# Kernel optimization log

Hardware: AMD Instinct MI355X
Metric: run time of the kernel (lower is better)

## Reference

```python
import jax, jax.numpy as jnp
import numpy as np

N_NODES = 8192
N_EDGES = 262144
D_FEAT = 512
NHID = 32
LATENT = 16


def setup_inputs() -> dict:
    key = jax.random.key(0)
    ks = jax.random.split(key, 12)
    inp = {
        "features": jax.random.normal(ks[0], (N_NODES, D_FEAT), dtype=jnp.float32),
        "edge_src": jax.random.randint(ks[1], (N_EDGES,), 0, N_NODES, dtype=jnp.int32),
        "edge_dst": jax.random.randint(ks[2], (N_EDGES,), 0, N_NODES, dtype=jnp.int32),
        "edge_weight": jax.random.uniform(ks[3], (N_EDGES,), dtype=jnp.float32),
        # GCEncoder params (GCNConv: out = A @ (x W) + b)
        "Wg1": jax.random.normal(ks[4], (D_FEAT, NHID), dtype=jnp.float32) / np.sqrt(D_FEAT),
        "bg1": jnp.zeros((NHID,), jnp.float32),
        "Wg2": jax.random.normal(ks[5], (NHID, LATENT), dtype=jnp.float32) / np.sqrt(NHID),
        "bg2": jnp.zeros((LATENT,), jnp.float32),
        # MLP encoder params
        "We1": jax.random.normal(ks[6], (D_FEAT, NHID), dtype=jnp.float32) / np.sqrt(D_FEAT),
        "be1": jnp.zeros((NHID,), jnp.float32),
        "We2": jax.random.normal(ks[7], (NHID, LATENT), dtype=jnp.float32) / np.sqrt(NHID),
        "be2": jnp.zeros((LATENT,), jnp.float32),
        # MLP decoder params (latent -> features)
        "Wd1": jax.random.normal(ks[8], (LATENT, NHID), dtype=jnp.float32) / np.sqrt(LATENT),
        "bd1": jnp.zeros((NHID,), jnp.float32),
        "Wd2": jax.random.normal(ks[9], (NHID, D_FEAT), dtype=jnp.float32) / np.sqrt(NHID),
        "bd2": jnp.zeros((D_FEAT,), jnp.float32),
    }
    return inp


def _gcn_conv(x, W, b, edge_src, edge_dst, edge_weight, n_nodes):
    # transform then sparse aggregate: A @ (x W) + b
    xw = x @ W                                   # [N, out]
    msg = xw[edge_src] * edge_weight[:, None]    # [E, out]
    agg = jax.ops.segment_sum(msg, edge_dst, num_segments=n_nodes)
    return agg + b


def reference(features, edge_src, edge_dst, edge_weight,
              Wg1, bg1, Wg2, bg2, We1, be1, We2, be2, Wd1, bd1, Wd2, bd2):
    n = features.shape[0]
    # GCEncoder (dropout p=0.0)
    h = jax.nn.relu(_gcn_conv(features, Wg1, bg1, edge_src, edge_dst, edge_weight, n))
    za = jax.nn.relu(_gcn_conv(h, Wg2, bg2, edge_src, edge_dst, edge_weight, n))
    # MLP encoder
    zx = jax.nn.relu(jax.nn.relu(features @ We1 + be1) @ We2 + be2)
    # concat latents
    z = jnp.concatenate([za, zx], axis=1)        # [N, 2*latent]
    # inner-product decoder: sigmoid(z z^T)  -> [N, N]
    adj_recon = jax.nn.sigmoid(z @ z.T)
    # feature decoder MLP
    feat_recon = jax.nn.relu(jax.nn.relu(zx @ Wd1 + bd1) @ Wd2 + bd2)
    return adj_recon, feat_recon, z
```

## Files before the change

kernel.cpp:

```cpp
#include <hip/hip_runtime.h>

typedef unsigned short ushort_t;
typedef __attribute__((ext_vector_type(8))) short short8;
typedef __attribute__((ext_vector_type(4))) float floatx4;

#define N_NODES 8192
#define N_EDGES 262144
#define D_FEAT 512
#define NHID 32
#define LATENT 16

#define ADJ_OFF 0
#define FEAT_OFF (8192*8192)
#define Z_OFF (8192*8192 + 8192*512)

static __device__ __forceinline__ ushort_t f2bf(float f) {
    unsigned int u = __float_as_uint(f);
    unsigned int r = u + 0x7fffu + ((u >> 16) & 1u);
    return (ushort_t)(r >> 16);
}

__global__ __launch_bounds__(256) void k_zero(int* counts) {
    int i = blockIdx.x * 256 + threadIdx.x;
    if (i < N_NODES) counts[i] = 0;
}

__global__ __launch_bounds__(256) void k_hist(const int* edst, int* counts) {
    int e = blockIdx.x * 256 + threadIdx.x;
    atomicAdd(&counts[edst[e]], 1);
}

__global__ __launch_bounds__(1024) void k_scan(const int* counts, int* offs, int* cursor) {
    __shared__ int sdata[1024];
    int t = threadIdx.x;
    int base = t * 8;
    int c[8], local[8];
    int s = 0;
    #pragma unroll
    for (int j = 0; j < 8; j++) { c[j] = counts[base + j]; }
    #pragma unroll
    for (int j = 0; j < 8; j++) { local[j] = s; s += c[j]; }
    sdata[t] = s;
    __syncthreads();
    for (int off = 1; off < 1024; off <<= 1) {
        int v = sdata[t];
        int add = (t >= off) ? sdata[t - off] : 0;
        __syncthreads();
        sdata[t] = v + add;
        __syncthreads();
    }
    int excl = (t == 0) ? 0 : sdata[t - 1];
    #pragma unroll
    for (int j = 0; j < 8; j++) {
        int o = excl + local[j];
        offs[base + j] = o;
        cursor[base + j] = o;
    }
}

__global__ __launch_bounds__(256) void k_scatter(const int* esrc, const int* edst,
                                                 const float* ew, int* cursor,
                                                 int* ssrc, float* sw) {
    int e = blockIdx.x * 256 + threadIdx.x;
    int d = edst[e];
    int pos = atomicAdd(&cursor[d], 1);
    ssrc[pos] = esrc[e];
    sw[pos] = ew[e];
}

__global__ __launch_bounds__(256) void k_enc(const float* feat, const float* Wg1,
                                             const float* We1, const float* be1,
                                             const float* We2, const float* be2,
                                             float* xwg, float* zxf) {
    __shared__ float WL[64][64];
    __shared__ float FL[32][68];
    __shared__ float HE[32][33];
    int tid = threadIdx.x;
    int n = tid >> 3;
    int c0 = (tid & 7) * 8;
    int m0 = blockIdx.x * 32;
    float acc[8];
    #pragma unroll
    for (int j = 0; j < 8; j++) acc[j] = 0.f;

    for (int kt = 0; kt < 8; kt++) {
        __syncthreads();
        for (int i = tid; i < 4096; i += 256) {
            int k = i >> 6, c = i & 63;
            int kg = kt * 64 + k;
            WL[k][c] = (c < 32) ? Wg1[kg * 32 + c] : We1[kg * 32 + (c - 32)];
        }
        {
            const float* src = feat + (m0 + n) * 512 + kt * 64 + c0;
            float4 v0 = *(const float4*)(src);
            float4 v1 = *(const float4*)(src + 4);
            *(float4*)&FL[n][c0] = v0;
            *(float4*)&FL[n][c0 + 4] = v1;
        }
        __syncthreads();
        #pragma unroll 4
        for (int k = 0; k < 64; k++) {
            float a = FL[n][k];
            float4 w0 = *(const float4*)&WL[k][c0];
            float4 w1 = *(const float4*)&WL[k][c0 + 4];
            acc[0] += a * w0.x; acc[1] += a * w0.y;
            acc[2] += a * w0.z; acc[3] += a * w0.w;
            acc[4] += a * w1.x; acc[5] += a * w1.y;
            acc[6] += a * w1.z; acc[7] += a * w1.w;
        }
    }
    if ((tid & 7) < 4) {
        #pragma unroll
        for (int j = 0; j < 8; j++) xwg[(m0 + n) * 32 + c0 + j] = acc[j];
    } else {
        int h0 = c0 - 32;
        #pragma unroll
        for (int j = 0; j < 8; j++) {
            float v = acc[j] + be1[h0 + j];
            HE[n][h0 + j] = v > 0.f ? v : 0.f;
        }
    }
    __syncthreads();
    int j0 = (tid & 7) * 2;
    #pragma unroll
    for (int jj = 0; jj < 2; jj++) {
        int j = j0 + jj;
        float s = be2[j];
        #pragma unroll 8
        for (int cc = 0; cc < 32; cc++) s += HE[n][cc] * We2[cc * 16 + j];
        zxf[(m0 + n) * 16 + j] = s > 0.f ? s : 0.f;
    }
}

__global__ __launch_bounds__(256) void k_agg1(const float* xwg, const int* offs,
                                              const int* counts, const int* ssrc,
                                              const float* sw, const float* bg1,
                                              const float* Wg2, float* hw2) {
    __shared__ float hsh[8][33];
    int ln = threadIdx.x >> 5, c = threadIdx.x & 31;
    int n = blockIdx.x * 8 + ln;
    int st = offs[n], en = st + counts[n];
    float acc = 0.f;
    for (int i = st; i < en; i++) {
        acc += sw[i] * xwg[ssrc[i] * 32 + c];
    }
    float h = acc + bg1[c];
    hsh[ln][c] = h > 0.f ? h : 0.f;
    __syncthreads();
    if (threadIdx.x < 128) {
        int l2 = threadIdx.x >> 4, j = threadIdx.x & 15;
        float s2 = 0.f;
        #pragma unroll 8
        for (int cc = 0; cc < 32; cc++) s2 += hsh[l2][cc] * Wg2[cc * 16 + j];
        hw2[(blockIdx.x * 8 + l2) * 16 + j] = s2;
    }
}

__global__ __launch_bounds__(256) void k_agg2(const float* hw2, const int* offs,
                                              const int* counts, const int* ssrc,
                                              const float* sw, const float* bg2,
                                              const float* zxf, ushort_t* zbf,
                                              float* zout) {
    int ln = threadIdx.x >> 4, c = threadIdx.x & 15;
    int n = blockIdx.x * 16 + ln;
    int st = offs[n], en = st + counts[n];
    float acc = 0.f;
    for (int i = st; i < en; i++) {
        acc += sw[i] * hw2[ssrc[i] * 16 + c];
    }
    float za = acc + bg2[c];
    za = za > 0.f ? za : 0.f;
    float zx = zxf[n * 16 + c];
    zout[n * 32 + c] = za;
    zout[n * 32 + 16 + c] = zx;
    zbf[n * 32 + c] = f2bf(za);
    zbf[n * 32 + 16 + c] = f2bf(zx);
}

__global__ __launch_bounds__(256) void k_feat1(const float* zxf, const float* Wd1,
                                               const float* bd1, float* tf) {
    int gid = blockIdx.x * 256 + threadIdx.x;
    int n = gid >> 5, c = gid & 31;
    float s = bd1[c];
    #pragma unroll
    for (int k = 0; k < 16; k++) s += zxf[n * 16 + k] * Wd1[k * 32 + c];
    tf[gid] = s > 0.f ? s : 0.f;
}

__global__ __launch_bounds__(256) void k_feat2(const float* tf, const float* Wd2,
                                               const float* bd2, float* outF) {
    int n = blockIdx.x;
    int c = threadIdx.x * 2;
    float s0 = bd2[c], s1 = bd2[c + 1];
    #pragma unroll 8
    for (int k = 0; k < 32; k++) {
        float t = tf[n * 32 + k];
        s0 += t * Wd2[k * 512 + c];
        s1 += t * Wd2[k * 512 + c + 1];
    }
    s0 = s0 > 0.f ? s0 : 0.f;
    s1 = s1 > 0.f ? s1 : 0.f;
    float2 pk = make_float2(s0, s1);
    *(float2*)(outF + n * 512 + c) = pk;
}

__global__ __launch_bounds__(256) void k_adj(const ushort_t* zbf, float* out) {
    int l = threadIdx.x & 63;
    int wv = threadIdx.x >> 6;
    int strip = blockIdx.x & 15;
    int rtg = blockIdx.x >> 4;
    int rt = rtg * 4 + wv;
    int q = l >> 4, cl = l & 15;
    int m0 = rt * 16, c0 = strip * 512;
    short8 a = *(const short8*)(zbf + (m0 + cl) * 32 + q * 8);
    for (int p = 0; p < 16; p++) {
        int colA = c0 + p * 32 + 2 * cl;
        short8 bA = *(const short8*)(zbf + colA * 32 + q * 8);
        short8 bB = *(const short8*)(zbf + (colA + 1) * 32 + q * 8);
        floatx4 accA = {0,0,0,0}, accB = {0,0,0,0};
        accA = __builtin_amdgcn_mfma_f32_16x16x32_bf16(a, bA, accA, 0, 0, 0);
        accB = __builtin_amdgcn_mfma_f32_16x16x32_bf16(a, bB, accB, 0, 0, 0);
        #pragma unroll
        for (int r = 0; r < 4; r++) {
            int row = m0 + q * 4 + r;
            float sA = 1.f / (1.f + __expf(-accA[r]));
            float sB = 1.f / (1.f + __expf(-accB[r]));
            float2 pk = make_float2(sA, sB);
            *(float2*)(out + (size_t)row * 8192 + colA) = pk;
        }
    }
}

extern "C" void kernel_launch(void* const* d_in, const int* in_sizes, int n_in,
                              void* d_out, int out_size, void* d_ws, size_t ws_size,
                              hipStream_t stream) {
    const float* feat = (const float*)d_in[0];
    const int* esrc = (const int*)d_in[1];
    const int* edst = (const int*)d_in[2];
    const float* ew = (const float*)d_in[3];
    const float* Wg1 = (const float*)d_in[4];
    const float* bg1 = (const float*)d_in[5];
    const float* Wg2 = (const float*)d_in[6];
    const float* bg2 = (const float*)d_in[7];
    const float* We1 = (const float*)d_in[8];
    const float* be1 = (const float*)d_in[9];
    const float* We2 = (const float*)d_in[10];
    const float* be2 = (const float*)d_in[11];
    const float* Wd1 = (const float*)d_in[12];
    const float* bd1 = (const float*)d_in[13];
    const float* Wd2 = (const float*)d_in[14];
    const float* bd2 = (const float*)d_in[15];
    float* out = (float*)d_out;

    char* ws = (char*)d_ws;
    float* xwg      = (float*)(ws + 0);
    float* zxf      = (float*)(ws + 1048576);
    float* hw2      = (float*)(ws + 1572864);
    ushort_t* zbf   = (ushort_t*)(ws + 2097152);
    float* tf       = (float*)(ws + 2621440);
    int* counts     = (int*)(ws + 3670016);
    int* offs       = (int*)(ws + 3702784);
    int* cursor     = (int*)(ws + 3735552);
    int* ssrc       = (int*)(ws + 3768320);
    float* sw       = (float*)(ws + 4816896);

    k_zero<<<32, 256, 0, stream>>>(counts);
    k_hist<<<N_EDGES / 256, 256, 0, stream>>>(edst, counts);
    k_scan<<<1, 1024, 0, stream>>>(counts, offs, cursor);
    k_scatter<<<N_EDGES / 256, 256, 0, stream>>>(esrc, edst, ew, cursor, ssrc, sw);
    k_enc<<<N_NODES / 32, 256, 0, stream>>>(feat, Wg1, We1, be1, We2, be2, xwg, zxf);
    k_agg1<<<N_NODES / 8, 256, 0, stream>>>(xwg, offs, counts, ssrc, sw, bg1, Wg2, hw2);
    k_agg2<<<N_NODES / 16, 256, 0, stream>>>(hw2, offs, counts, ssrc, sw, bg2, zxf,
                                             zbf, out + Z_OFF);
    k_feat1<<<N_NODES * 32 / 256, 256, 0, stream>>>(zxf, Wd1, bd1, tf);
    k_feat2<<<N_NODES, 256, 0, stream>>>(tf, Wd2, bd2, out + FEAT_OFF);
    k_adj<<<(N_NODES / 16 / 4) * 16, 256, 0, stream>>>(zbf, out + ADJ_OFF);
}
```

Baseline: 473.7 us.

## Pack edges, fuse feature decoder, widen adj stores with nontemporal writes

Packs edge source index and weight into one int2 array and unrolls the aggregation loops by four. Re-tiles the encoder GEMM and fuses the two feature-decoder kernels into one block that processes 16 nodes, writing with nontemporal stores. The adjacency kernel now computes four MFMA tiles per step so it can emit float4 nontemporal stores to the 256 MB output, aiming to improve write efficiency. Adds __restrict__ throughout; the trade-off is more registers per thread and more code complexity.

```diff
diff --git a/kernel.cpp b/kernel.cpp
--- a/kernel.cpp
+++ b/kernel.cpp
@@ -3,6 +3,7 @@
 typedef unsigned short ushort_t;
 typedef __attribute__((ext_vector_type(8))) short short8;
 typedef __attribute__((ext_vector_type(4))) float floatx4;
+typedef __attribute__((ext_vector_type(2))) float floatx2;
 
 #define N_NODES 8192
 #define N_EDGES 262144
@@ -20,17 +21,18 @@
     return (ushort_t)(r >> 16);
 }
 
-__global__ __launch_bounds__(256) void k_zero(int* counts) {
+__global__ __launch_bounds__(256) void k_zero(int* __restrict__ counts) {
     int i = blockIdx.x * 256 + threadIdx.x;
     if (i < N_NODES) counts[i] = 0;
 }
 
-__global__ __launch_bounds__(256) void k_hist(const int* edst, int* counts) {
+__global__ __launch_bounds__(256) void k_hist(const int* __restrict__ edst, int* __restrict__ counts) {
     int e = blockIdx.x * 256 + threadIdx.x;
     atomicAdd(&counts[edst[e]], 1);
 }
 
-__global__ __launch_bounds__(1024) void k_scan(const int* counts, int* offs, int* cursor) {
+__global__ __launch_bounds__(1024) void k_scan(const int* __restrict__ counts,
+                                               int* __restrict__ offs, int* __restrict__ cursor) {
     __shared__ int sdata[1024];
     int t = threadIdx.x;
     int base = t * 8;
@@ -58,91 +60,119 @@
     }
 }
 
-__global__ __launch_bounds__(256) void k_scatter(const int* esrc, const int* edst,
-                                                 const float* ew, int* cursor,
-                                                 int* ssrc, float* sw) {
+__global__ __launch_bounds__(256) void k_scatter(const int* __restrict__ esrc,
+                                                 const int* __restrict__ edst,
+                                                 const float* __restrict__ ew,
+                                                 int* __restrict__ cursor,
+                                                 int2* __restrict__ sedge) {
     int e = blockIdx.x * 256 + threadIdx.x;
     int d = edst[e];
     int pos = atomicAdd(&cursor[d], 1);
-    ssrc[pos] = esrc[e];
-    sw[pos] = ew[e];
-}
-
-__global__ __launch_bounds__(256) void k_enc(const float* feat, const float* Wg1,
-                                             const float* We1, const float* be1,
-                                             const float* We2, const float* be2,
-                                             float* xwg, float* zxf) {
-    __shared__ float WL[64][64];
-    __shared__ float FL[32][68];
+    sedge[pos] = make_int2(esrc[e], __float_as_int(ew[e]));
+}
+
+__global__ __launch_bounds__(256) void k_enc(const float* __restrict__ feat,
+                                             const float* __restrict__ Wg1,
+                                             const float* __restrict__ We1,
+                                             const float* __restrict__ be1,
+                                             const float* __restrict__ We2,
+                                             const float* __restrict__ be2,
+                                             float* __restrict__ xwg,
+                                             float* __restrict__ zxf) {
+    __shared__ float WL[32][64];
+    __shared__ float FL[32][33];
     __shared__ float HE[32][33];
     int tid = threadIdx.x;
-    int n = tid >> 3;
-    int c0 = (tid & 7) * 8;
+    int cr = tid & 15;
+    int nr = tid >> 4;
     int m0 = blockIdx.x * 32;
-    float acc[8];
-    #pragma unroll
-    for (int j = 0; j < 8; j++) acc[j] = 0.f;
-
-    for (int kt = 0; kt < 8; kt++) {
+    float acc[2][4] = {};
+
+    for (int kt = 0; kt < 16; kt++) {
         __syncthreads();
-        for (int i = tid; i < 4096; i += 256) {
-            int k = i >> 6, c = i & 63;
-            int kg = kt * 64 + k;
-            WL[k][c] = (c < 32) ? Wg1[kg * 32 + c] : We1[kg * 32 + (c - 32)];
-        }
         {
-            const float* src = feat + (m0 + n) * 512 + kt * 64 + c0;
-            float4 v0 = *(const float4*)(src);
-            float4 v1 = *(const float4*)(src + 4);
-            *(float4*)&FL[n][c0] = v0;
-            *(float4*)&FL[n][c0 + 4] = v1;
+            int i = tid;
+            #pragma unroll
+            for (int j = 0; j < 8; j++, i += 256) {
+                int k = i >> 6, c = i & 63;
+                int kg = kt * 32 + k;
+                WL[k][c] = (c < 32) ? Wg1[kg * 32 + c] : We1[kg * 32 + (c - 32)];
+            }
+        }
+        {
+            int n = tid >> 3, q = tid & 7;
+            float4 v = *(const float4*)(feat + (m0 + n) * 512 + kt * 32 + q * 4);
+            FL[n][q * 4 + 0] = v.x; FL[n][q * 4 + 1] = v.y;
+            FL[n][q * 4 + 2] = v.z; FL[n][q * 4 + 3] = v.w;
         }
         __syncthreads();
         #pragma unroll 4
-        for (int k = 0; k < 64; k++) {
-            float a = FL[n][k];
-            float4 w0 = *(const float4*)&WL[k][c0];
-            float4 w1 = *(const float4*)&WL[k][c0 + 4];
-            acc[0] += a * w0.x; acc[1] += a * w0.y;
-            acc[2] += a * w0.z; acc[3] += a * w0.w;
-            acc[4] += a * w1.x; acc[5] += a * w1.y;
-            acc[6] += a * w1.z; acc[7] += a * w1.w;
-        }
-    }
-    if ((tid & 7) < 4) {
-        #pragma unroll
-        for (int j = 0; j < 8; j++) xwg[(m0 + n) * 32 + c0 + j] = acc[j];
+        for (int k = 0; k < 32; k++) {
+            float4 w = *(const float4*)&WL[k][cr * 4];
+            float f0 = FL[nr * 2 + 0][k];
+            float f1 = FL[nr * 2 + 1][k];
+            acc[0][0] += f0 * w.x; acc[0][1] += f0 * w.y;
+            acc[0][2] += f0 * w.z; acc[0][3] += f0 * w.w;
+            acc[1][0] += f1 * w.x; acc[1][1] += f1 * w.y;
+            acc[1][2] += f1 * w.z; acc[1][3] += f1 * w.w;
+        }
+    }
+    int cg = cr * 4;
+    if (cg < 32) {
+        #pragma unroll
+        for (int j = 0; j < 2; j++) {
+            float4 v = make_float4(acc[j][0], acc[j][1], acc[j][2], acc[j][3]);
+            *(float4*)(xwg + (m0 + nr * 2 + j) * 32 + cg) = v;
+        }
     } else {
-        int h0 = c0 - 32;
-        #pragma unroll
-        for (int j = 0; j < 8; j++) {
-            float v = acc[j] + be1[h0 + j];
-            HE[n][h0 + j] = v > 0.f ? v : 0.f;
-        }
-    }
-    __syncthreads();
-    int j0 = (tid & 7) * 2;
-    #pragma unroll
-    for (int jj = 0; jj < 2; jj++) {
-        int j = j0 + jj;
-        float s = be2[j];
-        #pragma unroll 8
-        for (int cc = 0; cc < 32; cc++) s += HE[n][cc] * We2[cc * 16 + j];
-        zxf[(m0 + n) * 16 + j] = s > 0.f ? s : 0.f;
-    }
-}
-
-__global__ __launch_bounds__(256) void k_agg1(const float* xwg, const int* offs,
-                                              const int* counts, const int* ssrc,
-                                              const float* sw, const float* bg1,
-                                              const float* Wg2, float* hw2) {
+        int hc = cg - 32;
+        #pragma unroll
+        for (int j = 0; j < 2; j++) {
+            #pragma unroll
+            for (int t = 0; t < 4; t++) {
+                float v = acc[j][t] + be1[hc + t];
+                HE[nr * 2 + j][hc + t] = v > 0.f ? v : 0.f;
+            }
+        }
+    }
+    __syncthreads();
+    int n = tid >> 3, j0 = (tid & 7) * 2;
+    float s0 = be2[j0], s1 = be2[j0 + 1];
+    #pragma unroll 8
+    for (int cc = 0; cc < 32; cc++) {
+        float h = HE[n][cc];
+        s0 += h * We2[cc * 16 + j0];
+        s1 += h * We2[cc * 16 + j0 + 1];
+    }
+    s0 = s0 > 0.f ? s0 : 0.f;
+    s1 = s1 > 0.f ? s1 : 0.f;
+    *(float2*)(zxf + (m0 + n) * 16 + j0) = make_float2(s0, s1);
+}
+
+__global__ __launch_bounds__(256) void k_agg1(const float* __restrict__ xwg,
+                                              const int* __restrict__ offs,
+                                              const int* __restrict__ counts,
+                                              const int2* __restrict__ sedge,
+                                              const float* __restrict__ bg1,
+                                              const float* __restrict__ Wg2,
+                                              float* __restrict__ hw2) {
     __shared__ float hsh[8][33];
     int ln = threadIdx.x >> 5, c = threadIdx.x & 31;
     int n = blockIdx.x * 8 + ln;
     int st = offs[n], en = st + counts[n];
     float acc = 0.f;
-    for (int i = st; i < en; i++) {
-        acc += sw[i] * xwg[ssrc[i] * 32 + c];
+    int i = st;
+    for (; i + 4 <= en; i += 4) {
+        int2 e0 = sedge[i], e1 = sedge[i + 1], e2 = sedge[i + 2], e3 = sedge[i + 3];
+        float s0 = __int_as_float(e0.y) * xwg[e0.x * 32 + c];
+        float s1 = __int_as_float(e1.y) * xwg[e1.x * 32 + c];
+        float s2 = __int_as_float(e2.y) * xwg[e2.x * 32 + c];
+        float s3 = __int_as_float(e3.y) * xwg[e3.x * 32 + c];
+        acc += (s0 + s1) + (s2 + s3);
+    }
+    for (; i < en; i++) {
+        int2 e = sedge[i];
+        acc += __int_as_float(e.y) * xwg[e.x * 32 + c];
     }
     float h = acc + bg1[c];
     hsh[ln][c] = h > 0.f ? h : 0.f;
@@ -156,17 +186,30 @@
     }
 }
 
-__global__ __launch_bounds__(256) void k_agg2(const float* hw2, const int* offs,
-                                              const int* counts, const int* ssrc,
-                                              const float* sw, const float* bg2,
-                                              const float* zxf, ushort_t* zbf,
-                                              float* zout) {
+__global__ __launch_bounds__(256) void k_agg2(const float* __restrict__ hw2,
+                                              const int* __restrict__ offs,
+                                              const int* __restrict__ counts,
+                                              const int2* __restrict__ sedge,
+                                              const float* __restrict__ bg2,
+                                              const float* __restrict__ zxf,
+                                              ushort_t* __restrict__ zbf,
+                                              float* __restrict__ zout) {
     int ln = threadIdx.x >> 4, c = threadIdx.x & 15;
     int n = blockIdx.x * 16 + ln;
     int st = offs[n], en = st + counts[n];
     float acc = 0.f;
-    for (int i = st; i < en; i++) {
-        acc += sw[i] * hw2[ssrc[i] * 16 + c];
+    int i = st;
+    for (; i + 4 <= en; i += 4) {
+        int2 e0 = sedge[i], e1 = sedge[i + 1], e2 = sedge[i + 2], e3 = sedge[i + 3];
+        float s0 = __int_as_float(e0.y) * hw2[e0.x * 16 + c];
+        float s1 = __int_as_float(e1.y) * hw2[e1.x * 16 + c];
+        float s2 = __int_as_float(e2.y) * hw2[e2.x * 16 + c];
+        float s3 = __int_as_float(e3.y) * hw2[e3.x * 16 + c];
+        acc += (s0 + s1) + (s2 + s3);
+    }
+    for (; i < en; i++) {
+        int2 e = sedge[i];
+        acc += __int_as_float(e.y) * hw2[e.x * 16 + c];
     }
     float za = acc + bg2[c];
     za = za > 0.f ? za : 0.f;
@@ -177,56 +220,88 @@
     zbf[n * 32 + 16 + c] = f2bf(zx);
 }
 
-__global__ __launch_bounds__(256) void k_feat1(const float* zxf, const float* Wd1,
-                                               const float* bd1, float* tf) {
-    int gid = blockIdx.x * 256 + threadIdx.x;
-    int n = gid >> 5, c = gid & 31;
-    float s = bd1[c];
-    #pragma unroll
-    for (int k = 0; k < 16; k++) s += zxf[n * 16 + k] * Wd1[k * 32 + c];
-    tf[gid] = s > 0.f ? s : 0.f;
-}
-
-__global__ __launch_bounds__(256) void k_feat2(const float* tf, const float* Wd2,
-                                               const float* bd2, float* outF) {
-    int n = blockIdx.x;
-    int c = threadIdx.x * 2;
-    float s0 = bd2[c], s1 = bd2[c + 1];
-    #pragma unroll 8
+__global__ __launch_bounds__(256) void k_feat(const float* __restrict__ zxf,
+                                              const float* __restrict__ Wd1,
+                                              const float* __restrict__ bd1,
+                                              const float* __restrict__ Wd2,
+                                              const float* __restrict__ bd2,
+                                              float* __restrict__ outF) {
+    __shared__ float ZL[16][17];
+    __shared__ float HT[16][33];
+    int tid = threadIdx.x;
+    int m0 = blockIdx.x * 16;
+    {
+        int n = tid >> 4, k = tid & 15;
+        ZL[n][k] = zxf[(m0 + n) * 16 + k];
+    }
+    __syncthreads();
+    {
+        int o = tid * 2;
+        int n = o >> 5, c = o & 31;
+        float s0 = bd1[c], s1 = bd1[c + 1];
+        #pragma unroll
+        for (int k = 0; k < 16; k++) {
+            float z = ZL[n][k];
+            s0 += z * Wd1[k * 32 + c];
+            s1 += z * Wd1[k * 32 + c + 1];
+        }
+        HT[n][c] = s0 > 0.f ? s0 : 0.f;
+        HT[n][c + 1] = s1 > 0.f ? s1 : 0.f;
+    }
+    __syncthreads();
+    int c2 = tid * 2;
+    floatx2 acc[16];
+    #pragma unroll
+    for (int n = 0; n < 16; n++) acc[n] = (floatx2){0.f, 0.f};
     for (int k = 0; k < 32; k++) {
-        float t = tf[n * 32 + k];
-        s0 += t * Wd2[k * 512 + c];
-        s1 += t * Wd2[k * 512 + c + 1];
-    }
-    s0 = s0 > 0.f ? s0 : 0.f;
-    s1 = s1 > 0.f ? s1 : 0.f;
-    float2 pk = make_float2(s0, s1);
-    *(float2*)(outF + n * 512 + c) = pk;
-}
-
-__global__ __launch_bounds__(256) void k_adj(const ushort_t* zbf, float* out) {
+        float2 w = *(const float2*)(Wd2 + k * 512 + c2);
+        #pragma unroll
+        for (int n = 0; n < 16; n++) {
+            float t = HT[n][k];
+            acc[n].x += t * w.x;
+            acc[n].y += t * w.y;
+        }
+    }
+    float b0 = bd2[c2], b1 = bd2[c2 + 1];
+    #pragma unroll
+    for (int n = 0; n < 16; n++) {
+        float s0 = acc[n].x + b0, s1 = acc[n].y + b1;
+        s0 = s0 > 0.f ? s0 : 0.f;
+        s1 = s1 > 0.f ? s1 : 0.f;
+        floatx2 pk = {s0, s1};
+        __builtin_nontemporal_store(pk, (floatx2*)(outF + (size_t)(m0 + n) * 512 + c2));
+    }
+}
+
+__global__ __launch_bounds__(256) void k_adj(const ushort_t* __restrict__ zbf,
+                                             float* __restrict__ out) {
     int l = threadIdx.x & 63;
     int wv = threadIdx.x >> 6;
     int strip = blockIdx.x & 15;
-    int rtg = blockIdx.x >> 4;
-    int rt = rtg * 4 + wv;
+    int rt = (blockIdx.x >> 4) * 4 + wv;
     int q = l >> 4, cl = l & 15;
     int m0 = rt * 16, c0 = strip * 512;
     short8 a = *(const short8*)(zbf + (m0 + cl) * 32 + q * 8);
-    for (int p = 0; p < 16; p++) {
-        int colA = c0 + p * 32 + 2 * cl;
-        short8 bA = *(const short8*)(zbf + colA * 32 + q * 8);
-        short8 bB = *(const short8*)(zbf + (colA + 1) * 32 + q * 8);
-        floatx4 accA = {0,0,0,0}, accB = {0,0,0,0};
-        accA = __builtin_amdgcn_mfma_f32_16x16x32_bf16(a, bA, accA, 0, 0, 0);
-        accB = __builtin_amdgcn_mfma_f32_16x16x32_bf16(a, bB, accB, 0, 0, 0);
+    for (int g = 0; g < 8; g++) {
+        int cb = c0 + g * 64;
+        short8 b0 = *(const short8*)(zbf + (cb + 4 * cl + 0) * 32 + q * 8);
+        short8 b1 = *(const short8*)(zbf + (cb + 4 * cl + 1) * 32 + q * 8);
+        short8 b2 = *(const short8*)(zbf + (cb + 4 * cl + 2) * 32 + q * 8);
+        short8 b3 = *(const short8*)(zbf + (cb + 4 * cl + 3) * 32 + q * 8);
+        floatx4 zv = {0, 0, 0, 0};
+        floatx4 a0 = __builtin_amdgcn_mfma_f32_16x16x32_bf16(a, b0, zv, 0, 0, 0);
+        floatx4 a1 = __builtin_amdgcn_mfma_f32_16x16x32_bf16(a, b1, zv, 0, 0, 0);
+        floatx4 a2 = __builtin_amdgcn_mfma_f32_16x16x32_bf16(a, b2, zv, 0, 0, 0);
+        floatx4 a3 = __builtin_amdgcn_mfma_f32_16x16x32_bf16(a, b3, zv, 0, 0, 0);
         #pragma unroll
         for (int r = 0; r < 4; r++) {
+            floatx4 v;
+            v.x = 1.f / (1.f + __expf(-a0[r]));
+            v.y = 1.f / (1.f + __expf(-a1[r]));
+            v.z = 1.f / (1.f + __expf(-a2[r]));
+            v.w = 1.f / (1.f + __expf(-a3[r]));
             int row = m0 + q * 4 + r;
-            float sA = 1.f / (1.f + __expf(-accA[r]));
-            float sB = 1.f / (1.f + __expf(-accB[r]));
-            float2 pk = make_float2(sA, sB);
-            *(float2*)(out + (size_t)row * 8192 + colA) = pk;
+            __builtin_nontemporal_store(v, (floatx4*)(out + (size_t)row * 8192 + cb + 4 * cl));
         }
     }
 }
@@ -257,22 +332,19 @@
     float* zxf      = (float*)(ws + 1048576);
     float* hw2      = (float*)(ws + 1572864);
     ushort_t* zbf   = (ushort_t*)(ws + 2097152);
-    float* tf       = (float*)(ws + 2621440);
-    int* counts     = (int*)(ws + 3670016);
-    int* offs       = (int*)(ws + 3702784);
-    int* cursor     = (int*)(ws + 3735552);
-    int* ssrc       = (int*)(ws + 3768320);
-    float* sw       = (float*)(ws + 4816896);
+    int* counts     = (int*)(ws + 2621440);
+    int* offs       = (int*)(ws + 2654208);
+    int* cursor     = (int*)(ws + 2686976);
+    int2* sedge     = (int2*)(ws + 2719744);
 
     k_zero<<<32, 256, 0, stream>>>(counts);
     k_hist<<<N_EDGES / 256, 256, 0, stream>>>(edst, counts);
     k_scan<<<1, 1024, 0, stream>>>(counts, offs, cursor);
-    k_scatter<<<N_EDGES / 256, 256, 0, stream>>>(esrc, edst, ew, cursor, ssrc, sw);
+    k_scatter<<<N_EDGES / 256, 256, 0, stream>>>(esrc, edst, ew, cursor, sedge);
     k_enc<<<N_NODES / 32, 256, 0, stream>>>(feat, Wg1, We1, be1, We2, be2, xwg, zxf);
-    k_agg1<<<N_NODES / 8, 256, 0, stream>>>(xwg, offs, counts, ssrc, sw, bg1, Wg2, hw2);
-    k_agg2<<<N_NODES / 16, 256, 0, stream>>>(hw2, offs, counts, ssrc, sw, bg2, zxf,
+    k_agg1<<<N_NODES / 8, 256, 0, stream>>>(xwg, offs, counts, sedge, bg1, Wg2, hw2);
+    k_agg2<<<N_NODES / 16, 256, 0, stream>>>(hw2, offs, counts, sedge, bg2, zxf,
                                              zbf, out + Z_OFF);
-    k_feat1<<<N_NODES * 32 / 256, 256, 0, stream>>>(zxf, Wd1, bd1, tf);
-    k_feat2<<<N_NODES, 256, 0, stream>>>(tf, Wd2, bd2, out + FEAT_OFF);
+    k_feat<<<N_NODES / 16, 256, 0, stream>>>(zxf, Wd1, bd1, Wd2, bd2, out + FEAT_OFF);
     k_adj<<<(N_NODES / 16 / 4) * 16, 256, 0, stream>>>(zbf, out + ADJ_OFF);
 }
```

After: 454.7 us. 1.04x faster.
